# Optimization experiments

Hardware: AMD Instinct MI355X
Metric: run time of the kernel (lower is better)

Reference implementation:

```python
import jax, jax.numpy as jnp
import numpy as np

D_MODEL = 1024
N_HEADS = 16
D_HEAD = D_MODEL // N_HEADS
M_SLOPE = 0.5
BATCH = 2
SEQ = 2048


def setup_inputs() -> dict:
    key = jax.random.key(0)
    k1, k2, k3 = jax.random.split(key, 3)
    x = jax.random.normal(k1, (BATCH, SEQ, D_MODEL), dtype=jnp.float32)
    qkv_w = jax.random.normal(k2, (3 * D_MODEL, D_MODEL), dtype=jnp.float32) * (1.0 / np.sqrt(D_MODEL))
    qkv_b = jnp.zeros((3 * D_MODEL,), dtype=jnp.float32)
    out_w = jax.random.normal(k3, (D_MODEL, D_MODEL), dtype=jnp.float32) * (1.0 / np.sqrt(D_MODEL))
    out_b = jnp.zeros((D_MODEL,), dtype=jnp.float32)
    return {"x": x, "qkv_w": qkv_w, "qkv_b": qkv_b, "out_w": out_w, "out_b": out_b}


def _alibi_bias(n_heads, seq_len, m, dtype):
    # bias[h, i, j] = -|i - j| * m**h
    slopes = (m ** jnp.arange(n_heads, dtype=dtype))  # (H,)
    pos = jnp.arange(seq_len, dtype=dtype)
    dist = jnp.abs(pos[:, None] - pos[None, :])  # (S, S)
    return -dist[None, :, :] * slopes[:, None, None]  # (H, S, S)


def reference(x, qkv_w, qkv_b, out_w, out_b):
    batch, seq_len, d_model = x.shape
    qkv = x @ qkv_w.T + qkv_b  # (B, S, 3*D)
    qkv = qkv.reshape(batch, seq_len, N_HEADS, 3 * D_HEAD).transpose(0, 2, 1, 3)  # (B, H, S, 3*dh)
    q, k, v = jnp.split(qkv, 3, axis=-1)  # each (B, H, S, dh)
    scale = jnp.sqrt(jnp.asarray(D_HEAD, dtype=x.dtype))
    scores = jnp.einsum('bhid,bhjd->bhij', q, k) / scale  # (B, H, S, S)
    scores = scores + _alibi_bias(N_HEADS, seq_len, M_SLOPE, x.dtype)[None]
    attn = jax.nn.softmax(scores, axis=-1)
    out = jnp.einsum('bhij,bhjd->bhid', attn, v)  # (B, H, S, dh)
    out = out.transpose(0, 2, 1, 3).reshape(batch, seq_len, d_model)
    return out @ out_w.T + out_b
```

## Files before the change

kernel.cpp:

```cpp
#include <hip/hip_runtime.h>
#include <hip/hip_bf16.h>
#include <cstdint>
#include <cstddef>

typedef _Float16 half8 __attribute__((ext_vector_type(8)));
typedef _Float16 half4 __attribute__((ext_vector_type(4)));
typedef float floatx4 __attribute__((ext_vector_type(4)));

#define LOG2E 1.4426950408889634f

__device__ __forceinline__ void async_load16(const void* g, void* l) {
  void* gnc = const_cast<void*>(g);
  __builtin_amdgcn_global_load_lds(
      (__attribute__((address_space(1))) void*)(gnc),
      (__attribute__((address_space(3))) void*)(l), 16, 0, 0);
}

__global__ __launch_bounds__(256) void cvt_all(const float* __restrict__ x,
                                               const float* __restrict__ w1,
                                               const float* __restrict__ w2,
                                               _Float16* __restrict__ xh,
                                               _Float16* __restrict__ w1h,
                                               _Float16* __restrict__ w2h) {
  int i = blockIdx.x * 256 + threadIdx.x;
  const float* src;
  _Float16* dst;
  int off;
  if (i < 1048576) {
    src = x; dst = xh; off = i;
  } else if (i < 1048576 + 786432) {
    src = w1; dst = w1h; off = i - 1048576;
  } else {
    src = w2; dst = w2h; off = i - 1835008;
  }
  float4 v = reinterpret_cast<const float4*>(src)[off];
  half4 h = {(_Float16)v.x, (_Float16)v.y, (_Float16)v.z, (_Float16)v.w};
  reinterpret_cast<half4*>(dst)[off] = h;
}

__global__ __launch_bounds__(256) void qkv_gemm(const _Float16* __restrict__ X,
                                                const _Float16* __restrict__ W,
                                                const float* __restrict__ bias,
                                                _Float16* __restrict__ Q,
                                                _Float16* __restrict__ K,
                                                _Float16* __restrict__ V) {
  __shared__ _Float16 As[128 * 32];
  __shared__ _Float16 Bs[128 * 32];
  const int tid = threadIdx.x;
  const int lane = tid & 63, wid = tid >> 6;
  const int lr = lane & 15, lg = lane >> 4;
  const int bm = blockIdx.x, bn = blockIdx.y;
  const int wm = wid >> 1, wn = wid & 1;
  floatx4 acc[4][4] = {};

  for (int kt = 0; kt < 32; ++kt) {
    const int k0 = kt * 32;
    __syncthreads();
#pragma unroll
    for (int it = 0; it < 2; ++it) {
      int c = it * 256 + (wid << 6) + lane;
      int r = c >> 2, slot = c & 3;
      int cc = slot ^ ((r >> 1) & 3);
      async_load16(X + (size_t)(bm * 128 + r) * 1024 + k0 + cc * 8,
                   &As[(it * 256 + (wid << 6)) * 8]);
      async_load16(W + (size_t)(bn * 128 + r) * 1024 + k0 + cc * 8,
                   &Bs[(it * 256 + (wid << 6)) * 8]);
    }
    __syncthreads();
    half8 a[4], b[4];
#pragma unroll
    for (int mi = 0; mi < 4; ++mi) {
      int row = wm * 64 + mi * 16 + lr;
      int slot = lg ^ ((row >> 1) & 3);
      a[mi] = *(const half8*)&As[row * 32 + slot * 8];
    }
#pragma unroll
    for (int nj = 0; nj < 4; ++nj) {
      int row = wn * 64 + nj * 16 + lr;
      int slot = lg ^ ((row >> 1) & 3);
      b[nj] = *(const half8*)&Bs[row * 32 + slot * 8];
    }
#pragma unroll
    for (int mi = 0; mi < 4; ++mi)
#pragma unroll
      for (int nj = 0; nj < 4; ++nj)
        acc[mi][nj] = __builtin_amdgcn_mfma_f32_16x16x32_f16(a[mi], b[nj], acc[mi][nj], 0, 0, 0);
  }

#pragma unroll
  for (int nj = 0; nj < 4; ++nj) {
    int j = bn * 128 + wn * 64 + nj * 16 + lr;
    float bj = bias[j];
    int h = j / 192, rr = j % 192;
    int typ = rr >> 6, d = rr & 63;
    _Float16* dst = (typ == 0) ? Q : (typ == 1) ? K : V;
#pragma unroll
    for (int mi = 0; mi < 4; ++mi) {
#pragma unroll
      for (int r = 0; r < 4; ++r) {
        int i = bm * 128 + wm * 64 + mi * 16 + lg * 4 + r;
        int b_ = i >> 11, s = i & 2047;
        float v = acc[mi][nj][r] + bj;
        dst[(size_t)((b_ * 16 + h) * 2048 + s) * 64 + d] = (_Float16)v;
      }
    }
  }
}

__global__ __launch_bounds__(256) void transpose_v(const _Float16* __restrict__ V,
                                                   _Float16* __restrict__ Vt) {
  __shared__ _Float16 tile[64 * 80];
  const int t = threadIdx.x;
  const int s0 = blockIdx.x * 64;
  const int bh = blockIdx.y;
  const _Float16* src = V + (size_t)bh * 131072;
#pragma unroll
  for (int it = 0; it < 2; ++it) {
    int c = it * 256 + t;
    int rs = c >> 3, ch = c & 7;
    half8 v = *(const half8*)(src + (size_t)(s0 + rs) * 64 + ch * 8);
    *(half8*)&tile[rs * 80 + ch * 8] = v;
  }
  __syncthreads();
  _Float16* dst = Vt + (size_t)bh * 131072;
  int rd = t >> 2, cs = t & 3;
#pragma unroll
  for (int hf = 0; hf < 2; ++hf) {
    half8 v;
#pragma unroll
    for (int k = 0; k < 8; ++k) {
      int s = cs * 16 + hf * 8 + k;
      v[k] = tile[s * 80 + rd];
    }
    *(half8*)(dst + (size_t)rd * 2048 + s0 + cs * 16 + hf * 8) = v;
  }
}

__global__ __launch_bounds__(256, 4) void attn(const _Float16* __restrict__ Q,
                                               const _Float16* __restrict__ K,
                                               const _Float16* __restrict__ Vt,
                                               _Float16* __restrict__ O) {
  __shared__ _Float16 KPs[128 * 64];
  __shared__ _Float16 Vs[64 * 128];
  const int tid = threadIdx.x, lane = tid & 63, wid = tid >> 6;
  const int lr = lane & 15, lg = lane >> 4;
  const int qt = blockIdx.x, bh = blockIdx.y;
  const int h = bh & 15, b = bh >> 4;
  const int q0 = qt * 64 + wid * 16;
  const float slopeL2 = exp2f(-(float)h) * LOG2E;
  const float qscale = 0.125f * LOG2E;
  const float Mfix = 8.0f;
  const _Float16* Qg = Q + (size_t)bh * 131072;
  const _Float16* Kg = K + (size_t)bh * 131072;
  const _Float16* Vg = Vt + (size_t)bh * 131072;

  half8 qa[2];
#pragma unroll
  for (int kf = 0; kf < 2; ++kf)
    qa[kf] = *(const half8*)(Qg + (size_t)(q0 + lr) * 64 + kf * 32 + lg * 8);

  float lsum[4] = {0.f, 0.f, 0.f, 0.f};
  floatx4 o[4] = {};
  _Float16* Pw = &KPs[wid * 2048];
  const int ibase = q0 + lg * 4 - lr;

  for (int kt = 0; kt < 16; ++kt) {
    const int kv0 = kt * 128;
    __syncthreads();
#pragma unroll
    for (int it = 0; it < 4; ++it) {
      int c = it * 256 + (wid << 6) + lane;
      {
        int r = c >> 3, slot = c & 7, cc = slot ^ (r & 7);
        async_load16(Kg + (size_t)(kv0 + r) * 64 + cc * 8, &KPs[(it * 256 + (wid << 6)) * 8]);
      }
      {
        int r = c >> 4, slot = c & 15, cc = slot ^ (r & 15);
        async_load16(Vg + (size_t)r * 2048 + kv0 + cc * 8, &Vs[(it * 256 + (wid << 6)) * 8]);
      }
    }
    __syncthreads();

    floatx4 sc[8];
#pragma unroll
    for (int nj = 0; nj < 8; ++nj) sc[nj] = floatx4{0.f, 0.f, 0.f, 0.f};
#pragma unroll
    for (int nj = 0; nj < 8; ++nj) {
      int row = nj * 16 + lr;
#pragma unroll
      for (int kf = 0; kf < 2; ++kf) {
        int slot = (kf * 4 + lg) ^ (row & 7);
        half8 kb = *(const half8*)&KPs[row * 64 + slot * 8];
        sc[nj] = __builtin_amdgcn_mfma_f32_16x16x32_f16(qa[kf], kb, sc[nj], 0, 0, 0);
      }
    }
    __syncthreads();

#pragma unroll
    for (int r = 0; r < 4; ++r) {
      int prow = lg * 4 + r;
      float fj = (float)(ibase + r - kv0);
#pragma unroll
      for (int nj = 0; nj < 8; ++nj) {
        float t = fmaf(sc[nj][r], qscale, fmaf(fabsf(fj), -slopeL2, -Mfix));
        float p = __builtin_amdgcn_exp2f(t);
        lsum[r] += p;
        int col = nj * 16 + lr;
        int slot = (col >> 3) ^ (prow & 7);
        Pw[prow * 128 + slot * 8 + (col & 7)] = (_Float16)p;
        fj -= 16.0f;
      }
    }

#pragma unroll
    for (int kf2 = 0; kf2 < 4; ++kf2) {
      int slotp = (kf2 * 4 + lg) ^ (lr & 7);
      half8 pa = *(const half8*)&Pw[lr * 128 + slotp * 8];
#pragma unroll
      for (int nd = 0; nd < 4; ++nd) {
        int vrow = nd * 16 + lr;
        int slotv = (kf2 * 4 + lg) ^ (vrow & 15);
        half8 vb = *(const half8*)&Vs[vrow * 128 + slotv * 8];
        o[nd] = __builtin_amdgcn_mfma_f32_16x16x32_f16(pa, vb, o[nd], 0, 0, 0);
      }
    }
  }

#pragma unroll
  for (int r = 0; r < 4; ++r) {
#pragma unroll
    for (int x = 1; x < 16; x <<= 1) lsum[r] += __shfl_xor(lsum[r], x, 64);
  }
#pragma unroll
  for (int r = 0; r < 4; ++r) {
    float inv = 1.0f / lsum[r];
    int s = q0 + lg * 4 + r;
#pragma unroll
    for (int nd = 0; nd < 4; ++nd) {
      int d = nd * 16 + lr;
      O[((size_t)(b * 2048 + s)) * 1024 + h * 64 + d] = (_Float16)(o[nd][r] * inv);
    }
  }
}

__global__ __launch_bounds__(256) void out_gemm(const _Float16* __restrict__ A_,
                                                const _Float16* __restrict__ W,
                                                const float* __restrict__ bias,
                                                float* __restrict__ out) {
  __shared__ _Float16 As[128 * 32];
  __shared__ _Float16 Bs[128 * 32];
  const int tid = threadIdx.x;
  const int lane = tid & 63, wid = tid >> 6;
  const int lr = lane & 15, lg = lane >> 4;
  const int bm = blockIdx.x, bn = blockIdx.y;
  const int wm = wid >> 1, wn = wid & 1;
  floatx4 acc[4][4] = {};

  for (int kt = 0; kt < 32; ++kt) {
    const int k0 = kt * 32;
    __syncthreads();
#pragma unroll
    for (int it = 0; it < 2; ++it) {
      int c = it * 256 + (wid << 6) + lane;
      int r = c >> 2, slot = c & 3;
      int cc = slot ^ ((r >> 1) & 3);
      async_load16(A_ + (size_t)(bm * 128 + r) * 1024 + k0 + cc * 8,
                   &As[(it * 256 + (wid << 6)) * 8]);
      async_load16(W + (size_t)(bn * 128 + r) * 1024 + k0 + cc * 8,
                   &Bs[(it * 256 + (wid << 6)) * 8]);
    }
    __syncthreads();
    half8 a[4], b[4];
#pragma unroll
    for (int mi = 0; mi < 4; ++mi) {
      int row = wm * 64 + mi * 16 + lr;
      int slot = lg ^ ((row >> 1) & 3);
      a[mi] = *(const half8*)&As[row * 32 + slot * 8];
    }
#pragma unroll
    for (int nj = 0; nj < 4; ++nj) {
      int row = wn * 64 + nj * 16 + lr;
      int slot = lg ^ ((row >> 1) & 3);
      b[nj] = *(const half8*)&Bs[row * 32 + slot * 8];
    }
#pragma unroll
    for (int mi = 0; mi < 4; ++mi)
#pragma unroll
      for (int nj = 0; nj < 4; ++nj)
        acc[mi][nj] = __builtin_amdgcn_mfma_f32_16x16x32_f16(a[mi], b[nj], acc[mi][nj], 0, 0, 0);
  }

#pragma unroll
  for (int nj = 0; nj < 4; ++nj) {
    int j = bn * 128 + wn * 64 + nj * 16 + lr;
    float bj = bias[j];
#pragma unroll
    for (int mi = 0; mi < 4; ++mi) {
#pragma unroll
      for (int r = 0; r < 4; ++r) {
        int i = bm * 128 + wm * 64 + mi * 16 + lg * 4 + r;
        out[(size_t)i * 1024 + j] = acc[mi][nj][r] + bj;
      }
    }
  }
}

extern "C" void kernel_launch(void* const* d_in, const int* in_sizes, int n_in,
                              void* d_out, int out_size, void* d_ws, size_t ws_size,
                              hipStream_t stream) {
  const float* x = (const float*)d_in[0];
  const float* qkv_w = (const float*)d_in[1];
  const float* qkv_b = (const float*)d_in[2];
  const float* out_w = (const float*)d_in[3];
  const float* out_b = (const float*)d_in[4];
  float* out = (float*)d_out;
  char* ws = (char*)d_ws;

  _Float16* xh = (_Float16*)(ws + 0);
  _Float16* wqh = (_Float16*)(ws + 8388608);
  _Float16* woh = (_Float16*)(ws + 14680064);
  _Float16* Qh = (_Float16*)(ws + 16777216);
  _Float16* Kh = (_Float16*)(ws + 25165824);
  _Float16* Vh = (_Float16*)(ws + 33554432);
  _Float16* Vth = (_Float16*)(ws + 41943040);
  _Float16* Oh = (_Float16*)(ws + 50331648);

  cvt_all<<<8192, 256, 0, stream>>>(x, qkv_w, out_w, xh, wqh, woh);
  qkv_gemm<<<dim3(32, 24), 256, 0, stream>>>(xh, wqh, qkv_b, Qh, Kh, Vh);
  transpose_v<<<dim3(32, 32), 256, 0, stream>>>(Vh, Vth);
  attn<<<dim3(32, 32), 256, 0, stream>>>(Qh, Kh, Vth, Oh);
  out_gemm<<<dim3(32, 8), 256, 0, stream>>>(Oh, woh, out_b, out);
}
```

Baseline: 206.3 us.

## Double-buffer GEMM and attention tiles, fold Q scale, pack P stores

```diff
diff --git a/kernel.cpp b/kernel.cpp
--- a/kernel.cpp
+++ b/kernel.cpp
@@ -5,15 +5,21 @@
 
 typedef _Float16 half8 __attribute__((ext_vector_type(8)));
 typedef _Float16 half4 __attribute__((ext_vector_type(4)));
+typedef _Float16 half2v __attribute__((ext_vector_type(2)));
 typedef float floatx4 __attribute__((ext_vector_type(4)));
 
 #define LOG2E 1.4426950408889634f
+#define QSCALE (0.125f * LOG2E)
 
 __device__ __forceinline__ void async_load16(const void* g, void* l) {
   void* gnc = const_cast<void*>(g);
   __builtin_amdgcn_global_load_lds(
       (__attribute__((address_space(1))) void*)(gnc),
       (__attribute__((address_space(3))) void*)(l), 16, 0, 0);
+}
+
+__device__ __forceinline__ half2v cvt_pk_f16(float a, float b) {
+  return __builtin_bit_cast(half2v, __builtin_amdgcn_cvt_pkrtz(a, b));
 }
 
 __global__ __launch_bounds__(256) void cvt_all(const float* __restrict__ x,
@@ -44,8 +50,8 @@
                                                 _Float16* __restrict__ Q,
                                                 _Float16* __restrict__ K,
                                                 _Float16* __restrict__ V) {
-  __shared__ _Float16 As[128 * 32];
-  __shared__ _Float16 Bs[128 * 32];
+  __shared__ _Float16 As[2][128 * 64];
+  __shared__ _Float16 Bs[2][128 * 64];
   const int tid = threadIdx.x;
   const int lane = tid & 63, wid = tid >> 6;
   const int lr = lane & 15, lg = lane >> 4;
@@ -53,38 +59,48 @@
   const int wm = wid >> 1, wn = wid & 1;
   floatx4 acc[4][4] = {};
 
-  for (int kt = 0; kt < 32; ++kt) {
-    const int k0 = kt * 32;
-    __syncthreads();
-#pragma unroll
-    for (int it = 0; it < 2; ++it) {
+  auto stage = [&](int kt, int bsel) {
+    const int k0 = kt * 64;
+#pragma unroll
+    for (int it = 0; it < 4; ++it) {
       int c = it * 256 + (wid << 6) + lane;
-      int r = c >> 2, slot = c & 3;
-      int cc = slot ^ ((r >> 1) & 3);
+      int r = c >> 3, slot = c & 7;
+      int cc = slot ^ (r & 7);
       async_load16(X + (size_t)(bm * 128 + r) * 1024 + k0 + cc * 8,
-                   &As[(it * 256 + (wid << 6)) * 8]);
+                   &As[bsel][(it * 256 + (wid << 6)) * 8]);
       async_load16(W + (size_t)(bn * 128 + r) * 1024 + k0 + cc * 8,
-                   &Bs[(it * 256 + (wid << 6)) * 8]);
-    }
-    __syncthreads();
-    half8 a[4], b[4];
-#pragma unroll
-    for (int mi = 0; mi < 4; ++mi) {
-      int row = wm * 64 + mi * 16 + lr;
-      int slot = lg ^ ((row >> 1) & 3);
-      a[mi] = *(const half8*)&As[row * 32 + slot * 8];
-    }
-#pragma unroll
-    for (int nj = 0; nj < 4; ++nj) {
-      int row = wn * 64 + nj * 16 + lr;
-      int slot = lg ^ ((row >> 1) & 3);
-      b[nj] = *(const half8*)&Bs[row * 32 + slot * 8];
-    }
-#pragma unroll
-    for (int mi = 0; mi < 4; ++mi)
-#pragma unroll
-      for (int nj = 0; nj < 4; ++nj)
-        acc[mi][nj] = __builtin_amdgcn_mfma_f32_16x16x32_f16(a[mi], b[nj], acc[mi][nj], 0, 0, 0);
+                   &Bs[bsel][(it * 256 + (wid << 6)) * 8]);
+    }
+  };
+
+  stage(0, 0);
+  __syncthreads();
+
+  for (int kt = 0; kt < 16; ++kt) {
+    const int cur = kt & 1;
+    if (kt < 15) stage(kt + 1, cur ^ 1);
+#pragma unroll
+    for (int kf = 0; kf < 2; ++kf) {
+      half8 a[4], b[4];
+#pragma unroll
+      for (int mi = 0; mi < 4; ++mi) {
+        int row = wm * 64 + mi * 16 + lr;
+        int slot = (kf * 4 + lg) ^ (row & 7);
+        a[mi] = *(const half8*)&As[cur][row * 64 + slot * 8];
+      }
+#pragma unroll
+      for (int nj = 0; nj < 4; ++nj) {
+        int row = wn * 64 + nj * 16 + lr;
+        int slot = (kf * 4 + lg) ^ (row & 7);
+        b[nj] = *(const half8*)&Bs[cur][row * 64 + slot * 8];
+      }
+#pragma unroll
+      for (int mi = 0; mi < 4; ++mi)
+#pragma unroll
+        for (int nj = 0; nj < 4; ++nj)
+          acc[mi][nj] = __builtin_amdgcn_mfma_f32_16x16x32_f16(a[mi], b[nj], acc[mi][nj], 0, 0, 0);
+    }
+    if (kt < 15) __syncthreads();
   }
 
 #pragma unroll
@@ -93,6 +109,7 @@
     float bj = bias[j];
     int h = j / 192, rr = j % 192;
     int typ = rr >> 6, d = rr & 63;
+    float scl = (typ == 0) ? QSCALE : 1.0f;
     _Float16* dst = (typ == 0) ? Q : (typ == 1) ? K : V;
 #pragma unroll
     for (int mi = 0; mi < 4; ++mi) {
@@ -100,7 +117,7 @@
       for (int r = 0; r < 4; ++r) {
         int i = bm * 128 + wm * 64 + mi * 16 + lg * 4 + r;
         int b_ = i >> 11, s = i & 2047;
-        float v = acc[mi][nj][r] + bj;
+        float v = (acc[mi][nj][r] + bj) * scl;
         dst[(size_t)((b_ * 16 + h) * 2048 + s) * 64 + d] = (_Float16)v;
       }
     }
@@ -108,51 +125,48 @@
 }
 
 __global__ __launch_bounds__(256) void transpose_v(const _Float16* __restrict__ V,
-                                                   _Float16* __restrict__ Vt) {
-  __shared__ _Float16 tile[64 * 80];
+                                                   _Float16* __restrict__ Vp) {
+  __shared__ _Float16 tile[128 * 72];
   const int t = threadIdx.x;
-  const int s0 = blockIdx.x * 64;
+  const int s0 = blockIdx.x * 128;
   const int bh = blockIdx.y;
   const _Float16* src = V + (size_t)bh * 131072;
 #pragma unroll
-  for (int it = 0; it < 2; ++it) {
+  for (int it = 0; it < 4; ++it) {
     int c = it * 256 + t;
     int rs = c >> 3, ch = c & 7;
     half8 v = *(const half8*)(src + (size_t)(s0 + rs) * 64 + ch * 8);
-    *(half8*)&tile[rs * 80 + ch * 8] = v;
+    *(half8*)&tile[rs * 72 + ch * 8] = v;
   }
   __syncthreads();
-  _Float16* dst = Vt + (size_t)bh * 131072;
-  int rd = t >> 2, cs = t & 3;
-#pragma unroll
-  for (int hf = 0; hf < 2; ++hf) {
+  _Float16* dst = Vp + (size_t)bh * 131072;
+  const int rd = t >> 2, q4 = t & 3;
+#pragma unroll
+  for (int qq = 0; qq < 4; ++qq) {
     half8 v;
 #pragma unroll
-    for (int k = 0; k < 8; ++k) {
-      int s = cs * 16 + hf * 8 + k;
-      v[k] = tile[s * 80 + rd];
-    }
-    *(half8*)(dst + (size_t)rd * 2048 + s0 + cs * 16 + hf * 8) = v;
-  }
-}
-
-__global__ __launch_bounds__(256, 4) void attn(const _Float16* __restrict__ Q,
-                                               const _Float16* __restrict__ K,
-                                               const _Float16* __restrict__ Vt,
-                                               _Float16* __restrict__ O) {
-  __shared__ _Float16 KPs[128 * 64];
-  __shared__ _Float16 Vs[64 * 128];
+    for (int e = 0; e < 8; ++e) {
+      int u = e * 16 + q4 * 4 + qq;
+      v[e] = tile[u * 72 + rd];
+    }
+    *(half8*)(dst + (size_t)rd * 2048 + s0 + q4 * 32 + qq * 8) = v;
+  }
+}
+
+__global__ __launch_bounds__(256) void attn(const _Float16* __restrict__ Q,
+                                            const _Float16* __restrict__ K,
+                                            const _Float16* __restrict__ Vp,
+                                            _Float16* __restrict__ O) {
+  __shared__ _Float16 lds[40960];
   const int tid = threadIdx.x, lane = tid & 63, wid = tid >> 6;
   const int lr = lane & 15, lg = lane >> 4;
   const int qt = blockIdx.x, bh = blockIdx.y;
   const int h = bh & 15, b = bh >> 4;
   const int q0 = qt * 64 + wid * 16;
   const float slopeL2 = exp2f(-(float)h) * LOG2E;
-  const float qscale = 0.125f * LOG2E;
-  const float Mfix = 8.0f;
   const _Float16* Qg = Q + (size_t)bh * 131072;
   const _Float16* Kg = K + (size_t)bh * 131072;
-  const _Float16* Vg = Vt + (size_t)bh * 131072;
+  const _Float16* Vg = Vp + (size_t)bh * 131072;
 
   half8 qa[2];
 #pragma unroll
@@ -161,25 +175,31 @@
 
   float lsum[4] = {0.f, 0.f, 0.f, 0.f};
   floatx4 o[4] = {};
-  _Float16* Pw = &KPs[wid * 2048];
-  const int ibase = q0 + lg * 4 - lr;
-
-  for (int kt = 0; kt < 16; ++kt) {
+  _Float16* Pw = &lds[32768 + wid * 2048];
+
+  auto stage = [&](int kt, int bsel) {
     const int kv0 = kt * 128;
-    __syncthreads();
 #pragma unroll
     for (int it = 0; it < 4; ++it) {
       int c = it * 256 + (wid << 6) + lane;
-      {
-        int r = c >> 3, slot = c & 7, cc = slot ^ (r & 7);
-        async_load16(Kg + (size_t)(kv0 + r) * 64 + cc * 8, &KPs[(it * 256 + (wid << 6)) * 8]);
-      }
-      {
-        int r = c >> 4, slot = c & 15, cc = slot ^ (r & 15);
-        async_load16(Vg + (size_t)r * 2048 + kv0 + cc * 8, &Vs[(it * 256 + (wid << 6)) * 8]);
-      }
-    }
-    __syncthreads();
+      int rk = c >> 3, sk = c & 7, ck = sk ^ (rk & 7);
+      async_load16(Kg + (size_t)(kv0 + rk) * 64 + ck * 8,
+                   &lds[bsel * 8192 + (it * 256 + (wid << 6)) * 8]);
+      int rv = c >> 4, sv = c & 15, cv = sv ^ (rv & 15);
+      async_load16(Vg + (size_t)rv * 2048 + kv0 + cv * 8,
+                   &lds[16384 + bsel * 8192 + (it * 256 + (wid << 6)) * 8]);
+    }
+  };
+
+  stage(0, 0);
+  __syncthreads();
+
+  for (int kt = 0; kt < 16; ++kt) {
+    const int cur = kt & 1;
+    const int kv0 = kt * 128;
+    if (kt < 15) stage(kt + 1, cur ^ 1);
+    const _Float16* Kb = &lds[cur * 8192];
+    const _Float16* Vb = &lds[16384 + cur * 8192];
 
     floatx4 sc[8];
 #pragma unroll
@@ -190,40 +210,44 @@
 #pragma unroll
       for (int kf = 0; kf < 2; ++kf) {
         int slot = (kf * 4 + lg) ^ (row & 7);
-        half8 kb = *(const half8*)&KPs[row * 64 + slot * 8];
+        half8 kb = *(const half8*)&Kb[row * 64 + slot * 8];
         sc[nj] = __builtin_amdgcn_mfma_f32_16x16x32_f16(qa[kf], kb, sc[nj], 0, 0, 0);
       }
     }
-    __syncthreads();
-
+
+    const int ibase = q0 + lg * 4 - lr - kv0;
 #pragma unroll
     for (int r = 0; r < 4; ++r) {
-      int prow = lg * 4 + r;
-      float fj = (float)(ibase + r - kv0);
+      const int prow = lg * 4 + r;
+      float fj = (float)(ibase + r);
+      float p[8];
 #pragma unroll
       for (int nj = 0; nj < 8; ++nj) {
-        float t = fmaf(sc[nj][r], qscale, fmaf(fabsf(fj), -slopeL2, -Mfix));
-        float p = __builtin_amdgcn_exp2f(t);
-        lsum[r] += p;
-        int col = nj * 16 + lr;
-        int slot = (col >> 3) ^ (prow & 7);
-        Pw[prow * 128 + slot * 8 + (col & 7)] = (_Float16)p;
+        float t = fmaf(fabsf(fj), -slopeL2, sc[nj][r]);
+        p[nj] = __builtin_amdgcn_exp2f(t);
+        lsum[r] += p[nj];
         fj -= 16.0f;
       }
+      union { half8 h8; half2v h2[4]; } u;
+#pragma unroll
+      for (int c2 = 0; c2 < 4; ++c2)
+        u.h2[c2] = cvt_pk_f16(p[2 * c2], p[2 * c2 + 1]);
+      *(half8*)&Pw[prow * 128 + (lr ^ prow) * 8] = u.h8;
     }
 
 #pragma unroll
     for (int kf2 = 0; kf2 < 4; ++kf2) {
-      int slotp = (kf2 * 4 + lg) ^ (lr & 7);
+      int slotp = (kf2 * 4 + lg) ^ lr;
       half8 pa = *(const half8*)&Pw[lr * 128 + slotp * 8];
 #pragma unroll
       for (int nd = 0; nd < 4; ++nd) {
         int vrow = nd * 16 + lr;
         int slotv = (kf2 * 4 + lg) ^ (vrow & 15);
-        half8 vb = *(const half8*)&Vs[vrow * 128 + slotv * 8];
+        half8 vb = *(const half8*)&Vb[vrow * 128 + slotv * 8];
         o[nd] = __builtin_amdgcn_mfma_f32_16x16x32_f16(pa, vb, o[nd], 0, 0, 0);
       }
     }
+    if (kt < 15) __syncthreads();
   }
 
 #pragma unroll
@@ -247,8 +271,8 @@
                                                 const _Float16* __restrict__ W,
                                                 const float* __restrict__ bias,
                                                 float* __restrict__ out) {
-  __shared__ _Float16 As[128 * 32];
-  __shared__ _Float16 Bs[128 * 32];
+  __shared__ _Float16 As[2][128 * 64];
+  __shared__ _Float16 Bs[2][128 * 64];
   const int tid = threadIdx.x;
   const int lane = tid & 63, wid = tid >> 6;
   const int lr = lane & 15, lg = lane >> 4;
@@ -256,38 +280,48 @@
   const int wm = wid >> 1, wn = wid & 1;
   floatx4 acc[4][4] = {};
 
-  for (int kt = 0; kt < 32; ++kt) {
-    const int k0 = kt * 32;
-    __syncthreads();
-#pragma unroll
-    for (int it = 0; it < 2; ++it) {
+  auto stage = [&](int kt, int bsel) {
+    const int k0 = kt * 64;
+#pragma unroll
+    for (int it = 0; it < 4; ++it) {
       int c = it * 256 + (wid << 6) + lane;
-      int r = c >> 2, slot = c & 3;
-      int cc = slot ^ ((r >> 1) & 3);
+      int r = c >> 3, slot = c & 7;
+      int cc = slot ^ (r & 7);
       async_load16(A_ + (size_t)(bm * 128 + r) * 1024 + k0 + cc * 8,
-                   &As[(it * 256 + (wid << 6)) * 8]);
+                   &As[bsel][(it * 256 + (wid << 6)) * 8]);
       async_load16(W + (size_t)(bn * 128 + r) * 1024 + k0 + cc * 8,
-                   &Bs[(it * 256 + (wid << 6)) * 8]);
-    }
-    __syncthreads();
-    half8 a[4], b[4];
-#pragma unroll
-    for (int mi = 0; mi < 4; ++mi) {
-      int row = wm * 64 + mi * 16 + lr;
-      int slot = lg ^ ((row >> 1) & 3);
-      a[mi] = *(const half8*)&As[row * 32 + slot * 8];
-    }
-#pragma unroll
-    for (int nj = 0; nj < 4; ++nj) {
-      int row = wn * 64 + nj * 16 + lr;
-      int slot = lg ^ ((row >> 1) & 3);
-      b[nj] = *(const half8*)&Bs[row * 32 + slot * 8];
-    }
-#pragma unroll
-    for (int mi = 0; mi < 4; ++mi)
-#pragma unroll
-      for (int nj = 0; nj < 4; ++nj)
-        acc[mi][nj] = __builtin_amdgcn_mfma_f32_16x16x32_f16(a[mi], b[nj], acc[mi][nj], 0, 0, 0);
+                   &Bs[bsel][(it * 256 + (wid << 6)) * 8]);
+    }
+  };
+
+  stage(0, 0);
+  __syncthreads();
+
+  for (int kt = 0; kt < 16; ++kt) {
+    const int cur = kt & 1;
+    if (kt < 15) stage(kt + 1, cur ^ 1);
+#pragma unroll
+    for (int kf = 0; kf < 2; ++kf) {
+      half8 a[4], b[4];
+#pragma unroll
+      for (int mi = 0; mi < 4; ++mi) {
+        int row = wm * 64 + mi * 16 + lr;
+        int slot = (kf * 4 + lg) ^ (row & 7);
+        a[mi] = *(const half8*)&As[cur][row * 64 + slot * 8];
+      }
+#pragma unroll
+      for (int nj = 0; nj < 4; ++nj) {
+        int row = wn * 64 + nj * 16 + lr;
+        int slot = (kf * 4 + lg) ^ (row & 7);
+        b[nj] = *(const half8*)&Bs[cur][row * 64 + slot * 8];
+      }
+#pragma unroll
+      for (int mi = 0; mi < 4; ++mi)
+#pragma unroll
+        for (int nj = 0; nj < 4; ++nj)
+          acc[mi][nj] = __builtin_amdgcn_mfma_f32_16x16x32_f16(a[mi], b[nj], acc[mi][nj], 0, 0, 0);
+    }
+    if (kt < 15) __syncthreads();
   }
 
 #pragma unroll
@@ -322,12 +356,12 @@
   _Float16* Qh = (_Float16*)(ws + 16777216);
   _Float16* Kh = (_Float16*)(ws + 25165824);
   _Float16* Vh = (_Float16*)(ws + 33554432);
-  _Float16* Vth = (_Float16*)(ws + 41943040);
+  _Float16* Vph = (_Float16*)(ws + 41943040);
   _Float16* Oh = (_Float16*)(ws + 50331648);
 
   cvt_all<<<8192, 256, 0, stream>>>(x, qkv_w, out_w, xh, wqh, woh);
   qkv_gemm<<<dim3(32, 24), 256, 0, stream>>>(xh, wqh, qkv_b, Qh, Kh, Vh);
-  transpose_v<<<dim3(32, 32), 256, 0, stream>>>(Vh, Vth);
-  attn<<<dim3(32, 32), 256, 0, stream>>>(Qh, Kh, Vth, Oh);
+  transpose_v<<<dim3(16, 32), 256, 0, stream>>>(Vh, Vph);
+  attn<<<dim3(32, 32), 256, 0, stream>>>(Qh, Kh, Vph, Oh);
   out_gemm<<<dim3(32, 8), 256, 0, stream>>>(Oh, woh, out_b, out);
 }
```

Result: slower. 211.6 us (+2.6%).
